# Kernel tuning notes

Hardware: AMD Instinct MI355X
Metric: run time of the kernel (lower is better)

The kernel has to match this reference:

```python
import jax, jax.numpy as jnp
import numpy as np

N = 50000      # nodes
E = 800000     # edges
IN_DIM = 256
H = 128
OUT_DIM = 64
DEPTH = 3
NEG_SLOPE = 0.2  # DGL GATConv default leaky_relu slope


def setup_inputs() -> dict:
    key = jax.random.key(0)
    ks = jax.random.split(key, 20)
    def nrm(k, shape, fan_in):
        return jax.random.normal(k, shape, jnp.float32) / jnp.sqrt(jnp.float32(fan_in))
    x = jax.random.normal(ks[0], (N, IN_DIM), jnp.float32)
    src = jax.random.randint(ks[1], (E,), 0, N, jnp.int32)
    dst = jax.random.randint(ks[2], (E,), 0, N, jnp.int32)
    # weights stored as [in, out] (y = x @ W + b)
    inp = dict(
        x=x, src=src, dst=dst,
        wx_W=nrm(ks[3], (IN_DIM, H), IN_DIM), wx_b=jnp.zeros((H,), jnp.float32),
        gat_W=nrm(ks[4], (DEPTH, H, H), H), gat_b=jnp.zeros((DEPTH, H), jnp.float32),
        attn_l=nrm(ks[5], (DEPTH, H), H), attn_r=nrm(ks[6], (DEPTH, H), H),
        ig_W=nrm(ks[7], (DEPTH, 2 * H, H), 2 * H), ig_b=jnp.zeros((DEPTH, H), jnp.float32),
        fg_W=nrm(ks[8], (DEPTH, 2 * H, H), 2 * H), fg_b=jnp.zeros((DEPTH, H), jnp.float32),
        og_W=nrm(ks[9], (DEPTH, 2 * H, H), 2 * H), og_b=jnp.zeros((DEPTH, H), jnp.float32),
        st_W=nrm(ks[10], (DEPTH, 2 * H, H), 2 * H), st_b=jnp.zeros((DEPTH, H), jnp.float32),
        out_W=nrm(ks[11], (H, OUT_DIM), H), out_b=jnp.zeros((OUT_DIM,), jnp.float32),
    )
    return inp


def _breadth(h, W, b, a_l, a_r, src, dst):
    """DGL GATConv with 1 head + tanh activation; mean over heads is identity."""
    z = h @ W                                  # [N, H]
    el = z @ a_l                               # [N]
    er = z @ a_r                               # [N]
    e = jax.nn.leaky_relu(el[src] + er[dst], NEG_SLOPE)   # [E]
    # edge softmax over incoming edges of each dst node
    emax = jax.ops.segment_max(e, dst, num_segments=N)    # [N]
    emax = jnp.where(jnp.isfinite(emax), emax, 0.0)       # guard isolated nodes
    ex = jnp.exp(e - emax[dst])                            # [E]
    denom = jax.ops.segment_sum(ex, dst, num_segments=N)   # [N]
    alpha = ex / jnp.maximum(denom, 1e-16)[dst]             # [E]
    agg = jax.ops.segment_sum(alpha[:, None] * z[src], dst, num_segments=N)  # [N, H]
    return jnp.tanh(agg + b)


def reference(x, src, dst, wx_W, wx_b, gat_W, gat_b, attn_l, attn_r,
              ig_W, ig_b, fg_W, fg_b, og_W, og_b, st_W, st_b, out_W, out_b):
    h0 = x @ wx_W + wx_b                       # [N, H]
    h = h0
    collector = []
    for i in range(DEPTH):
        h = _breadth(h, gat_W[i], gat_b[i], attn_l[i], attn_r[i], src, dst)
        collector.append(h)
    mu = h0
    c = jnp.zeros_like(mu)
    for i in range(DEPTH):
        hm = jnp.concatenate([collector[i], mu], axis=1)   # [N, 2H]
        ig = jax.nn.sigmoid(hm @ ig_W[i] + ig_b[i])
        fg = jax.nn.sigmoid(hm @ fg_W[i] + fg_b[i])
        og = jax.nn.sigmoid(hm @ og_W[i] + og_b[i])
        c_tilde = jnp.tanh(hm @ st_W[i] + st_b[i])
        c = fg * c + ig * c_tilde
        mu = og * jnp.tanh(c)
    return jax.nn.relu(mu @ out_W + out_b)     # [N, OUT_DIM]
```

## Files before the change

### kernel.cpp

```cpp
#include <hip/hip_runtime.h>
#include <math.h>
#include <type_traits>

#define NN 50000
#define EE 800000
#define IN_D 256
#define HH 128
#define OUT_D 64
#define DEPTH 3
#define BK 512
#define NBK 98

typedef unsigned short u16;
typedef __bf16  bf16x8 __attribute__((ext_vector_type(8)));
typedef short   short8 __attribute__((ext_vector_type(8)));
typedef float   f32x4  __attribute__((ext_vector_type(4)));

__device__ __forceinline__ u16 f2b(float f){
    unsigned u = __float_as_uint(f);
    u += 0x7fff + ((u>>16)&1);
    return (u16)(u>>16);
}
__device__ __forceinline__ float b2f(u16 h){ return __uint_as_float(((unsigned)h)<<16); }

#define LOG2E 1.4426950408889634f
#if __has_builtin(__builtin_amdgcn_exp2f)
__device__ __forceinline__ float fexp2(float x){ return __builtin_amdgcn_exp2f(x); }
#else
__device__ __forceinline__ float fexp2(float x){ return exp2f(x); }
#endif
#if __has_builtin(__builtin_amdgcn_rcpf)
__device__ __forceinline__ float frcp(float x){ return __builtin_amdgcn_rcpf(x); }
#else
__device__ __forceinline__ float frcp(float x){ return 1.f/x; }
#endif
__device__ __forceinline__ float sigm(float x){ return frcp(1.f + fexp2(-x*LOG2E)); }
__device__ __forceinline__ float ftanh(float x){
    float ax = fabsf(x);
    float u = fexp2(ax * (-2.f*LOG2E));
    float r = (1.f - u) * frcp(1.f + u);
    return copysignf(r, x);
}

enum { EPI_BF=0, EPI_RELU=1, EPI_ZEL=2, EPI_GATES_FIRST=3, EPI_GATES=4 };

template<int EPI, int WAVES, int CT, int K, typename TA>
__global__ __launch_bounds__(WAVES*64, 4) void rgemm_k(
    const TA* __restrict__ A1, const u16* __restrict__ A2,
    const u16* __restrict__ Bp,
    const float* __restrict__ b1, const float* __restrict__ b2,
    const float* __restrict__ b3, const float* __restrict__ b4,
    void* __restrict__ Out, float* __restrict__ aux1, float* __restrict__ aux2,
    int Nrows)
{
    constexpr int TH = WAVES*64;
    constexpr int KS = K/32;
    constexpr int M  = WAVES*CT*16;
    constexpr bool GATES = (EPI==EPI_GATES || EPI==EPI_GATES_FIRST);
    __shared__ u16 As[64*K];
    __shared__ float elp[(EPI==EPI_ZEL)?64*WAVES:1];
    __shared__ float erp[(EPI==EPI_ZEL)?64*WAVES:1];

    const int tid = threadIdx.x;
    const int rb  = blockIdx.x*64;

    constexpr int CHUNKS = 64*K/(TH*8);
    #pragma unroll
    for (int c = 0; c < CHUNKS; ++c) {
        int h = (tid + c*TH)*8;
        int row = h / K, kk = h % K;
        int grow = rb + row; if (grow >= Nrows) grow = Nrows-1;
        short8 v;
        if constexpr (std::is_same<TA,float>::value) {
            const float* p = (const float*)A1 + (size_t)grow*K + kk;
            float4 x0 = *(const float4*)p;
            float4 x1 = *(const float4*)(p+4);
            v[0]=(short)f2b(x0.x); v[1]=(short)f2b(x0.y); v[2]=(short)f2b(x0.z); v[3]=(short)f2b(x0.w);
            v[4]=(short)f2b(x1.x); v[5]=(short)f2b(x1.y); v[6]=(short)f2b(x1.z); v[7]=(short)f2b(x1.w);
        } else if constexpr (GATES) {
            const u16* p = (kk < HH) ? ((const u16*)A1 + (size_t)grow*HH + kk)
                                     : (A2 + (size_t)grow*HH + (kk-HH));
            v = *(const short8*)p;
        } else {
            v = *(const short8*)((const u16*)A1 + (size_t)grow*K + kk);
        }
        int byte = row*(K*2) + ((kk*2) ^ ((row&7)<<4));
        *(short8*)((char*)As + byte) = v;
    }
    __syncthreads();

    const int lane = tid & 63, w = tid >> 6;
    const int ml = lane & 15, ksel = lane >> 4;
    f32x4 acc[4][CT] = {};
    #pragma unroll
    for (int ks = 0; ks < KS; ++ks) {
        bf16x8 a[4];
        #pragma unroll
        for (int rt = 0; rt < 4; ++rt) {
            int row = rt*16 + ml;
            int byte = row*(K*2) + (((ks*32 + ksel*8)*2) ^ ((row&7)<<4));
            a[rt] = *(const bf16x8*)((const char*)As + byte);
        }
        #pragma unroll
        for (int j = 0; j < CT; ++j) {
            int ctg = j*WAVES + w;
            bf16x8 b = *(const bf16x8*)(Bp + (((size_t)(ctg*KS + ks))<<9) + lane*8);
            #pragma unroll
            for (int rt = 0; rt < 4; ++rt)
                acc[rt][j] = __builtin_amdgcn_mfma_f32_16x16x32_bf16(a[rt], b, acc[rt][j], 0,0,0);
        }
    }

    if constexpr (EPI==EPI_BF || EPI==EPI_RELU) {
        #pragma unroll
        for (int rt = 0; rt < 4; ++rt)
        #pragma unroll
        for (int r = 0; r < 4; ++r) {
            int row = rb + rt*16 + ksel*4 + r;
            if (row >= Nrows) continue;
            #pragma unroll
            for (int j = 0; j < CT; ++j) {
                int gc = (j*WAVES + w)*16 + ml;
                float vv = acc[rt][j][r] + b1[gc];
                if (EPI==EPI_BF) ((u16*)Out)[(size_t)row*M + gc]   = f2b(vv);
                else             ((float*)Out)[(size_t)row*M + gc] = fmaxf(vv, 0.f);
            }
        }
    } else if constexpr (EPI==EPI_ZEL) {
        float pel[4][4] = {}, per[4][4] = {};
        #pragma unroll
        for (int j = 0; j < CT; ++j) {
            int gc = (j*WAVES + w)*16 + ml;
            float alc = b1[gc], arc = b2[gc];
            #pragma unroll
            for (int rt = 0; rt < 4; ++rt)
            #pragma unroll
            for (int r = 0; r < 4; ++r) {
                int row = rb + rt*16 + ksel*4 + r;
                float vv = acc[rt][j][r];
                if (row < Nrows) ((u16*)Out)[(size_t)row*HH + gc] = f2b(vv);
                pel[rt][r] = fmaf(vv, alc, pel[rt][r]);
                per[rt][r] = fmaf(vv, arc, per[rt][r]);
            }
        }
        #pragma unroll
        for (int msk = 1; msk < 16; msk <<= 1)
            #pragma unroll
            for (int rt = 0; rt < 4; ++rt)
            #pragma unroll
            for (int r = 0; r < 4; ++r) {
                pel[rt][r] += __shfl_xor(pel[rt][r], msk);
                per[rt][r] += __shfl_xor(per[rt][r], msk);
            }
        if (ml == 0) {
            #pragma unroll
            for (int rt = 0; rt < 4; ++rt)
            #pragma unroll
            for (int r = 0; r < 4; ++r) {
                int lr = rt*16 + ksel*4 + r;
                elp[lr*WAVES + w] = pel[rt][r];
                erp[lr*WAVES + w] = per[rt][r];
            }
        }
        __syncthreads();
        if (tid < 64) {
            int row = rb + tid;
            if (row < Nrows) {
                float s1 = 0.f, s2 = 0.f;
                #pragma unroll
                for (int wv = 0; wv < WAVES; ++wv) { s1 += elp[tid*WAVES+wv]; s2 += erp[tid*WAVES+wv]; }
                aux1[row] = s1; aux2[row] = s2;
            }
        }
    } else {
        #pragma unroll
        for (int rt = 0; rt < 4; ++rt)
        #pragma unroll
        for (int r = 0; r < 4; ++r) {
            int row = rb + rt*16 + ksel*4 + r;
            if (row >= Nrows) continue;
            int gcg = w*16 + ml;
            size_t o = (size_t)row*HH + gcg;
            float ig = sigm (acc[rt][0][r] + b1[gcg]);
            float st = ftanh(acc[rt][1][r] + b2[gcg]);
            float fg = sigm (acc[rt][2][r] + b3[gcg]);
            float og = sigm (acc[rt][3][r] + b4[gcg]);
            float P  = ig * st;
            float cn = (EPI==EPI_GATES_FIRST) ? P : fmaf(fg, aux1[o], P);
            aux1[o] = cn;
            ((u16*)Out)[o] = f2b(og * ftanh(cn));
        }
    }
}

struct PK  { const float* s; u16* d; int K; int Mc; };
struct PKs { PK t[17]; };
__global__ __launch_bounds__(256) void pack_k(PKs ps){
    const PK t = ps.t[blockIdx.y];
    int o = blockIdx.x*256 + threadIdx.x;
    if (o >= t.K * t.Mc) return;
    int i = o & 7, lane = (o>>3) & 63, rst = o >> 9;
    int KS = t.K >> 5;
    int ks = rst % KS, ct = rst / KS;
    int col = ct*16 + (lane & 15);
    int k   = ks*32 + (lane>>4)*8 + i;
    t.d[o] = f2b(t.s[(size_t)k*t.Mc + col]);
}

__global__ __launch_bounds__(256) void binh_k(const int* __restrict__ dst, int* __restrict__ bcnt){
    __shared__ int h[NBK];
    int t = threadIdx.x;
    if (t < NBK) h[t] = 0;
    __syncthreads();
    int base = blockIdx.x*4096;
    #pragma unroll
    for (int c = 0; c < 16; ++c){ int e = base + c*256 + t; if (e < EE) atomicAdd(&h[dst[e]>>9], 1); }
    __syncthreads();
    if (t < NBK && h[t]) atomicAdd(&bcnt[t], h[t]);
}
__global__ __launch_bounds__(128) void bscan_k(const int* __restrict__ bcnt,
                                               int* __restrict__ bbase, int* __restrict__ gcur){
    __shared__ int s[128];
    int t = threadIdx.x;
    int v = (t < NBK) ? bcnt[t] : 0;
    s[t] = v; __syncthreads();
    for (int off=1; off<128; off<<=1){ int x = (t>=off)? s[t-off] : 0; __syncthreads(); s[t] += x; __syncthreads(); }
    if (t < NBK){ bbase[t] = s[t]-v; gcur[t] = s[t]-v; }
}
__global__ __launch_bounds__(256) void binsc_k(const int* __restrict__ dst, const int* __restrict__ src,
                                               int* __restrict__ gcur, unsigned* __restrict__ staged){
    __shared__ int h[NBK], bb[NBK], lc[NBK];
    int t = threadIdx.x;
    if (t < NBK){ h[t]=0; lc[t]=0; }
    __syncthreads();
    int base = blockIdx.x*4096;
    int d[16], s[16];
    #pragma unroll
    for (int c = 0; c < 16; ++c){
        int e = base + c*256 + t; d[c] = -1;
        if (e < EE){ d[c] = dst[e]; s[c] = src[e]; atomicAdd(&h[d[c]>>9], 1); }
    }
    __syncthreads();
    if (t < NBK && h[t]) bb[t] = atomicAdd(&gcur[t], h[t]);
    __syncthreads();
    #pragma unroll
    for (int c = 0; c < 16; ++c) if (d[c] >= 0){
        int b = d[c]>>9;
        int r = atomicAdd(&lc[b], 1);
        staged[bb[b] + r] = ((unsigned)(d[c] & 511) << 16) | (unsigned)s[c];
    }
}
__global__ __launch_bounds__(BK) void build_k(const int* __restrict__ bcnt, const int* __restrict__ bbase,
                                              const unsigned* __restrict__ staged,
                                              int* __restrict__ rp, int* __restrict__ deg, u16* __restrict__ srcs){
    __shared__ int soff[BK], cur[BK];
    int t = threadIdx.x, bk = blockIdx.x;
    int n0 = bk*BK;
    soff[t] = 0; cur[t] = 0;
    __syncthreads();
    int cb = bcnt[bk], eb = bbase[bk];
    for (int j = t; j < cb; j += BK) atomicAdd(&soff[staged[eb+j]>>16], 1);
    __syncthreads();
    int d0 = soff[t];
    for (int off=1; off<BK; off<<=1){ int x = (t>=off)? soff[t-off] : 0; __syncthreads(); soff[t] += x; __syncthreads(); }
    int ex = soff[t] - d0;
    __syncthreads();
    soff[t] = ex;
    int n = n0 + t;
    if (n < NN){ deg[n] = d0; rp[n] = eb + ex; }
    __syncthreads();
    for (int j = t; j < cb; j += BK){
        unsigned p = staged[eb+j];
        int l = p >> 16;
        int r = atomicAdd(&cur[l], 1);
        srcs[eb + soff[l] + r] = (u16)(p & 0xffff);
    }
}

__global__ __launch_bounds__(256) void gat_k(
    const u16* __restrict__ z, const float* __restrict__ el, const float* __restrict__ er,
    const u16* __restrict__ srcs, const int* __restrict__ rp, const int* __restrict__ deg,
    const float* __restrict__ bias, u16* __restrict__ hout)
{
    int n = blockIdx.x*4 + (threadIdx.x>>6);
    if (n >= NN) return;
    int lane = threadIdx.x & 63;
    int start = rp[n], cnt = deg[n];
    float ern = er[n];
    const int slot = lane >> 4;
    const int ch   = (lane & 15) * 8;
    float acc[8] = {};

    if (cnt <= 64) {
        float v = -1e30f; int s_reg = 0;
        if (lane < cnt) {
            s_reg = srcs[start + lane];
            float tv = el[s_reg] + ern;
            v = tv >= 0.f ? tv : 0.2f*tv;
        }
        float m = v;
        #pragma unroll
        for (int off=1; off<64; off<<=1) m = fmaxf(m, __shfl_xor(m, off));
        float a = (lane < cnt) ? fexp2((v - m)*LOG2E) : 0.f;
        float ss = a;
        #pragma unroll
        for (int off=1; off<64; off<<=1) ss += __shfl_xor(ss, off);
        float a_reg = a * frcp(fmaxf(ss, 1e-16f));

        const int cntp = (cnt + 7) & ~7;
        for (int i = slot; i < cntp; i += 8) {
            float w0 = __shfl(a_reg, i),   w1 = __shfl(a_reg, i+4);
            int   s0 = __shfl(s_reg, i),   s1 = __shfl(s_reg, i+4);
            short8 v0 = *(const short8*)(z + (size_t)s0*HH + ch);
            short8 v1 = *(const short8*)(z + (size_t)s1*HH + ch);
            #pragma unroll
            for (int j=0;j<8;j++) acc[j] = fmaf(w1, b2f((u16)v1[j]), fmaf(w0, b2f((u16)v0[j]), acc[j]));
        }
    } else {
        float m = -1e30f;
        for (int i=lane; i<cnt; i+=64){ float tv = el[srcs[start+i]] + ern; tv = tv>=0.f?tv:0.2f*tv; m = fmaxf(m, tv); }
        #pragma unroll
        for (int off=1; off<64; off<<=1) m = fmaxf(m, __shfl_xor(m, off));
        float ss = 0.f;
        for (int i=lane; i<cnt; i+=64){ float tv = el[srcs[start+i]] + ern; tv = tv>=0.f?tv:0.2f*tv; ss += fexp2((tv-m)*LOG2E); }
        #pragma unroll
        for (int off=1; off<64; off<<=1) ss += __shfl_xor(ss, off);
        float inv = frcp(fmaxf(ss, 1e-16f));
        for (int i=slot; i<cnt; i+=4) {
            int sn = srcs[start+i];
            float tv = el[sn] + ern; tv = tv>=0.f?tv:0.2f*tv;
            float w0 = fexp2((tv-m)*LOG2E) * inv;
            short8 v0 = *(const short8*)(z + (size_t)sn*HH + ch);
            #pragma unroll
            for (int j=0;j<8;j++) acc[j] = fmaf(w0, b2f((u16)v0[j]), acc[j]);
        }
    }
    #pragma unroll
    for (int j=0;j<8;j++){ acc[j] += __shfl_xor(acc[j],16); acc[j] += __shfl_xor(acc[j],32); }
    if (slot == 0) {
        short8 o8;
        #pragma unroll
        for (int j=0;j<8;j++) o8[j] = (short)f2b(ftanh(acc[j] + bias[ch+j]));
        *(short8*)(hout + (size_t)n*HH + ch) = o8;
    }
}

extern "C" void kernel_launch(void* const* d_in, const int* in_sizes, int n_in,
                              void* d_out, int out_size, void* d_ws, size_t ws_size,
                              hipStream_t stream)
{
    const float* x    = (const float*)d_in[0];
    const int*   src  = (const int*)d_in[1];
    const int*   dst  = (const int*)d_in[2];
    const float* wxW  = (const float*)d_in[3];
    const float* wxb  = (const float*)d_in[4];
    const float* gatW = (const float*)d_in[5];
    const float* gatb = (const float*)d_in[6];
    const float* attl = (const float*)d_in[7];
    const float* attr = (const float*)d_in[8];
    const float* igW  = (const float*)d_in[9];
    const float* igb  = (const float*)d_in[10];
    const float* fgW  = (const float*)d_in[11];
    const float* fgb  = (const float*)d_in[12];
    const float* ogW  = (const float*)d_in[13];
    const float* ogb  = (const float*)d_in[14];
    const float* stW  = (const float*)d_in[15];
    const float* stb  = (const float*)d_in[16];
    const float* outW = (const float*)d_in[17];
    const float* outb = (const float*)d_in[18];

    char* w = (char*)d_ws;
    auto alloc = [&](size_t bytes)->char* { char* p = w; w += (bytes + 255) & ~(size_t)255; return p; };
    const size_t NH = (size_t)NN * HH;
    u16*      muB    = (u16*)alloc(NH*2);
    u16*      zB     = (u16*)alloc(NH*2);
    u16*      coll0  = (u16*)alloc(NH*2);
    u16*      coll1  = (u16*)alloc(NH*2);
    u16*      coll2  = (u16*)alloc(NH*2);
    float*    cbuf   = (float*)alloc(NH*4);
    float*    el     = (float*)alloc((size_t)NN*4);
    float*    er     = (float*)alloc((size_t)NN*4);
    unsigned* staged = (unsigned*)alloc((size_t)EE*4);
    u16*      srcs   = (u16*)alloc((size_t)EE*2);
    int*      deg    = (int*)alloc((size_t)NN*4);
    int*      rp     = (int*)alloc((size_t)NN*4);
    int*      bcnt   = (int*)alloc(128*4);
    int*      bbase  = (int*)alloc(128*4);
    int*      gcur   = (int*)alloc(128*4);
    u16*      bpool  = (u16*)alloc(483328*2);
    u16* wxP   = bpool;
    u16* gatP  = bpool + 32768;
    u16* gateP = bpool + 81920;
    u16* outP  = bpool + 475136;
    u16* coll[3] = {coll0, coll1, coll2};

    PKs ps;
    ps.t[0] = {wxW, wxP, IN_D, HH};
    for (int i=0;i<3;i++) ps.t[1+i]  = {gatW + (size_t)i*HH*HH,   gatP  + i*16384,           HH,   HH};
    for (int i=0;i<3;i++) ps.t[4+i]  = {igW  + (size_t)i*2*HH*HH, gateP + i*131072,          2*HH, HH};
    for (int i=0;i<3;i++) ps.t[7+i]  = {stW  + (size_t)i*2*HH*HH, gateP + i*131072 + 32768,  2*HH, HH};
    for (int i=0;i<3;i++) ps.t[10+i] = {fgW  + (size_t)i*2*HH*HH, gateP + i*131072 + 65536,  2*HH, HH};
    for (int i=0;i<3;i++) ps.t[13+i] = {ogW  + (size_t)i*2*HH*HH, gateP + i*131072 + 98304,  2*HH, HH};
    ps.t[16] = {outW, outP, HH, OUT_D};
    pack_k<<<dim3(128,17), 256, 0, stream>>>(ps);

    hipMemsetAsync(bcnt, 0, 128*4, stream);
    const int gE = (EE + 4095) / 4096;
    binh_k <<<gE, 256, 0, stream>>>(dst, bcnt);
    bscan_k<<<1, 128, 0, stream>>>(bcnt, bbase, gcur);
    binsc_k<<<gE, 256, 0, stream>>>(dst, src, gcur, staged);
    build_k<<<NBK, BK, 0, stream>>>(bcnt, bbase, staged, rp, deg, srcs);

    const int gN = (NN + 63) / 64;
    const int gA = (NN + 3) / 4;

    rgemm_k<EPI_BF,4,2,IN_D,float><<<gN, 256, 0, stream>>>(
        x, nullptr, wxP, wxb, nullptr, nullptr, nullptr, muB, nullptr, nullptr, NN);

    const u16* hin = muB;
    for (int i = 0; i < DEPTH; ++i) {
        rgemm_k<EPI_ZEL,4,2,HH,u16><<<gN, 256, 0, stream>>>(
            hin, nullptr, gatP + i*16384, attl + i*HH, attr + i*HH, nullptr, nullptr,
            zB, el, er, NN);
        gat_k<<<gA, 256, 0, stream>>>(zB, el, er, srcs, rp, deg, gatb + i*HH, coll[i]);
        hin = coll[i];
    }

    rgemm_k<EPI_GATES_FIRST,8,4,2*HH,u16><<<gN, 512, 0, stream>>>(
        coll[0], muB, gateP, igb, stb, fgb, ogb, muB, cbuf, nullptr, NN);
    for (int i = 1; i < DEPTH; ++i)
        rgemm_k<EPI_GATES,8,4,2*HH,u16><<<gN, 512, 0, stream>>>(
            coll[i], muB, gateP + i*131072, igb + i*HH, stb + i*HH, fgb + i*HH, ogb + i*HH,
            muB, cbuf, nullptr, NN);

    rgemm_k<EPI_RELU,4,1,HH,u16><<<gN, 256, 0, stream>>>(
        muB, nullptr, outP, outb, nullptr, nullptr, nullptr, (float*)d_out, nullptr, nullptr, NN);
}
```

Before: 328.4 us.

## Fuse the three LSTM-style gate GEMM layers into one kernel

Replaces the three separate gate GEMM launches with one kernel that processes all depth steps for a 64-row tile. The cell state stays in registers and mu stays in shared memory, so the fp32 cell-state buffer and the intermediate mu writes and reads to global memory go away. Each block now keeps two 16KB shared tiles and runs its steps in sequence, which may lower occupancy. It also adds syncs between steps.

```diff
diff --git a/kernel.cpp b/kernel.cpp
--- a/kernel.cpp
+++ b/kernel.cpp
@@ -42,21 +42,19 @@
     return copysignf(r, x);
 }
 
-enum { EPI_BF=0, EPI_RELU=1, EPI_ZEL=2, EPI_GATES_FIRST=3, EPI_GATES=4 };
+enum { EPI_BF=0, EPI_RELU=1, EPI_ZEL=2 };
 
 template<int EPI, int WAVES, int CT, int K, typename TA>
 __global__ __launch_bounds__(WAVES*64, 4) void rgemm_k(
-    const TA* __restrict__ A1, const u16* __restrict__ A2,
+    const TA* __restrict__ A1,
     const u16* __restrict__ Bp,
     const float* __restrict__ b1, const float* __restrict__ b2,
-    const float* __restrict__ b3, const float* __restrict__ b4,
     void* __restrict__ Out, float* __restrict__ aux1, float* __restrict__ aux2,
     int Nrows)
 {
     constexpr int TH = WAVES*64;
     constexpr int KS = K/32;
     constexpr int M  = WAVES*CT*16;
-    constexpr bool GATES = (EPI==EPI_GATES || EPI==EPI_GATES_FIRST);
     __shared__ u16 As[64*K];
     __shared__ float elp[(EPI==EPI_ZEL)?64*WAVES:1];
     __shared__ float erp[(EPI==EPI_ZEL)?64*WAVES:1];
@@ -77,10 +75,6 @@
             float4 x1 = *(const float4*)(p+4);
             v[0]=(short)f2b(x0.x); v[1]=(short)f2b(x0.y); v[2]=(short)f2b(x0.z); v[3]=(short)f2b(x0.w);
             v[4]=(short)f2b(x1.x); v[5]=(short)f2b(x1.y); v[6]=(short)f2b(x1.z); v[7]=(short)f2b(x1.w);
-        } else if constexpr (GATES) {
-            const u16* p = (kk < HH) ? ((const u16*)A1 + (size_t)grow*HH + kk)
-                                     : (A2 + (size_t)grow*HH + (kk-HH));
-            v = *(const short8*)p;
         } else {
             v = *(const short8*)((const u16*)A1 + (size_t)grow*K + kk);
         }
@@ -126,7 +120,7 @@
                 else             ((float*)Out)[(size_t)row*M + gc] = fmaxf(vv, 0.f);
             }
         }
-    } else if constexpr (EPI==EPI_ZEL) {
+    } else {
         float pel[4][4] = {}, per[4][4] = {};
         #pragma unroll
         for (int j = 0; j < CT; ++j) {
@@ -172,23 +166,98 @@
                 aux1[row] = s1; aux2[row] = s2;
             }
         }
-    } else {
+    }
+}
+
+__global__ __launch_bounds__(512, 4) void depth_k(
+    const u16* __restrict__ coll0, const u16* __restrict__ coll1, const u16* __restrict__ coll2,
+    u16* __restrict__ mu,
+    const u16* __restrict__ gateP,
+    const float* __restrict__ igb, const float* __restrict__ stb,
+    const float* __restrict__ fgb, const float* __restrict__ ogb,
+    int Nrows)
+{
+    __shared__ u16 As[64*HH];
+    __shared__ u16 Ms[64*HH];
+    const int tid = threadIdx.x;
+    const int rb  = blockIdx.x*64;
+    const int lane = tid & 63, w = tid >> 6;
+    const int ml = lane & 15, ksel = lane >> 4;
+    const int gcg = w*16 + ml;
+
+    #pragma unroll
+    for (int c = 0; c < 2; ++c) {
+        int h = (tid + c*512)*8;
+        int row = h >> 7, kk = h & 127;
+        int grow = rb + row; if (grow >= Nrows) grow = Nrows-1;
+        short8 v = *(const short8*)(mu + (size_t)grow*HH + kk);
+        *(short8*)((char*)Ms + row*256 + ((kk*2) ^ ((row&7)<<4))) = v;
+    }
+
+    float cc[4][4];
+    const u16* colls[3] = {coll0, coll1, coll2};
+
+    for (int i = 0; i < DEPTH; ++i) {
+        const u16* coll = colls[i];
+        #pragma unroll
+        for (int c = 0; c < 2; ++c) {
+            int h = (tid + c*512)*8;
+            int row = h >> 7, kk = h & 127;
+            int grow = rb + row; if (grow >= Nrows) grow = Nrows-1;
+            short8 v = *(const short8*)(coll + (size_t)grow*HH + kk);
+            *(short8*)((char*)As + row*256 + ((kk*2) ^ ((row&7)<<4))) = v;
+        }
+        __syncthreads();
+
+        f32x4 acc[4][4] = {};
+        #pragma unroll
+        for (int ks = 0; ks < 8; ++ks) {
+            const char* Sb = (ks < 4) ? (const char*)As : (const char*)Ms;
+            int kk2 = ((ks & 3)*32 + ksel*8)*2;
+            bf16x8 a[4];
+            #pragma unroll
+            for (int rt = 0; rt < 4; ++rt) {
+                int row = rt*16 + ml;
+                a[rt] = *(const bf16x8*)(Sb + row*256 + (kk2 ^ ((row&7)<<4)));
+            }
+            #pragma unroll
+            for (int j = 0; j < 4; ++j) {
+                bf16x8 b = *(const bf16x8*)(gateP + (size_t)i*131072 + (j*8 + w)*4096 + ks*512 + lane*8);
+                #pragma unroll
+                for (int rt = 0; rt < 4; ++rt)
+                    acc[rt][j] = __builtin_amdgcn_mfma_f32_16x16x32_bf16(a[rt], b, acc[rt][j], 0,0,0);
+            }
+        }
+        __syncthreads();
+
+        float bi = igb[i*HH + gcg], bs = stb[i*HH + gcg];
+        float bf_ = fgb[i*HH + gcg], bo = ogb[i*HH + gcg];
         #pragma unroll
         for (int rt = 0; rt < 4; ++rt)
         #pragma unroll
         for (int r = 0; r < 4; ++r) {
-            int row = rb + rt*16 + ksel*4 + r;
-            if (row >= Nrows) continue;
-            int gcg = w*16 + ml;
-            size_t o = (size_t)row*HH + gcg;
-            float ig = sigm (acc[rt][0][r] + b1[gcg]);
-            float st = ftanh(acc[rt][1][r] + b2[gcg]);
-            float fg = sigm (acc[rt][2][r] + b3[gcg]);
-            float og = sigm (acc[rt][3][r] + b4[gcg]);
+            float ig = sigm (acc[rt][0][r] + bi);
+            float st = ftanh(acc[rt][1][r] + bs);
+            float fg = sigm (acc[rt][2][r] + bf_);
+            float og = sigm (acc[rt][3][r] + bo);
             float P  = ig * st;
-            float cn = (EPI==EPI_GATES_FIRST) ? P : fmaf(fg, aux1[o], P);
-            aux1[o] = cn;
-            ((u16*)Out)[o] = f2b(og * ftanh(cn));
+            float cn = (i == 0) ? P : fmaf(fg, cc[rt][r], P);
+            cc[rt][r] = cn;
+            float mun = og * ftanh(cn);
+            int lrow = rt*16 + ksel*4 + r;
+            *(u16*)((char*)Ms + lrow*256 + ((gcg*2) ^ ((lrow&7)<<4))) = f2b(mun);
+        }
+        __syncthreads();
+    }
+
+    #pragma unroll
+    for (int c = 0; c < 2; ++c) {
+        int h = (tid + c*512)*8;
+        int row = h >> 7, kk = h & 127;
+        int grow = rb + row;
+        if (grow < Nrows) {
+            short8 v = *(const short8*)((const char*)Ms + row*256 + ((kk*2) ^ ((row&7)<<4)));
+            *(short8*)(mu + (size_t)grow*HH + kk) = v;
         }
     }
 }
@@ -377,7 +446,6 @@
     u16*      coll0  = (u16*)alloc(NH*2);
     u16*      coll1  = (u16*)alloc(NH*2);
     u16*      coll2  = (u16*)alloc(NH*2);
-    float*    cbuf   = (float*)alloc(NH*4);
     float*    el     = (float*)alloc((size_t)NN*4);
     float*    er     = (float*)alloc((size_t)NN*4);
     unsigned* staged = (unsigned*)alloc((size_t)EE*4);
@@ -415,24 +483,19 @@
     const int gA = (NN + 3) / 4;
 
     rgemm_k<EPI_BF,4,2,IN_D,float><<<gN, 256, 0, stream>>>(
-        x, nullptr, wxP, wxb, nullptr, nullptr, nullptr, muB, nullptr, nullptr, NN);
+        x, wxP, wxb, nullptr, muB, nullptr, nullptr, NN);
 
     const u16* hin = muB;
     for (int i = 0; i < DEPTH; ++i) {
         rgemm_k<EPI_ZEL,4,2,HH,u16><<<gN, 256, 0, stream>>>(
-            hin, nullptr, gatP + i*16384, attl + i*HH, attr + i*HH, nullptr, nullptr,
-            zB, el, er, NN);
+            hin, gatP + i*16384, attl + i*HH, attr + i*HH, zB, el, er, NN);
         gat_k<<<gA, 256, 0, stream>>>(zB, el, er, srcs, rp, deg, gatb + i*HH, coll[i]);
         hin = coll[i];
     }
 
-    rgemm_k<EPI_GATES_FIRST,8,4,2*HH,u16><<<gN, 512, 0, stream>>>(
-        coll[0], muB, gateP, igb, stb, fgb, ogb, muB, cbuf, nullptr, NN);
-    for (int i = 1; i < DEPTH; ++i)
-        rgemm_k<EPI_GATES,8,4,2*HH,u16><<<gN, 512, 0, stream>>>(
-            coll[i], muB, gateP + i*131072, igb + i*HH, stb + i*HH, fgb + i*HH, ogb + i*HH,
-            muB, cbuf, nullptr, NN);
+    depth_k<<<gN, 512, 0, stream>>>(coll0, coll1, coll2, muB, gateP,
+                                    igb, stb, fgb, ogb, NN);
 
     rgemm_k<EPI_RELU,4,1,HH,u16><<<gN, 256, 0, stream>>>(
-        muB, nullptr, outP, outb, nullptr, nullptr, nullptr, (float*)d_out, nullptr, nullptr, NN);
-}
+        muB, outP, outb, nullptr, (float*)d_out, nullptr, nullptr, NN);
+}
```

After: 321.0 us. -2.3%, faster.
